# Kernel tuning notes

Hardware: AMD Instinct MI355X
Metric: run time of the kernel (lower is better)

The kernel has to match this reference:

```python
import jax, jax.numpy as jnp
import numpy as np

D_MODEL = 768
D_STATE = 16
B, L = 4, 2048


def setup_inputs() -> dict:
    key = jax.random.key(0)
    ks = jax.random.split(key, 8)
    s = 1.0 / np.sqrt(D_MODEL)
    x = jax.random.normal(ks[0], (B, L, D_MODEL), jnp.float32)
    W_in = jax.random.normal(ks[1], (D_MODEL, 2 * D_MODEL), jnp.float32) * s
    b_in = jnp.zeros((2 * D_MODEL,), jnp.float32)
    W_B = jax.random.normal(ks[2], (D_MODEL, D_STATE), jnp.float32) * s
    b_B = jnp.zeros((D_STATE,), jnp.float32)
    W_C = jax.random.normal(ks[3], (D_MODEL, D_STATE), jnp.float32) * s
    b_C = jnp.zeros((D_STATE,), jnp.float32)
    W_delta = jax.random.normal(ks[4], (D_MODEL, D_MODEL), jnp.float32) * s
    b_delta = jnp.zeros((D_MODEL,), jnp.float32)
    W_out = jax.random.normal(ks[5], (D_MODEL, D_MODEL), jnp.float32) * s
    b_out = jnp.zeros((D_MODEL,), jnp.float32)
    # A_log init from the module: log(A + 1) with A[s, d] = s+1
    A_log = jnp.log(jnp.arange(1, D_STATE + 1, dtype=jnp.float32)[:, None]
                    * jnp.ones((1, D_MODEL), jnp.float32) + 1.0)
    D = jnp.ones((D_MODEL,), jnp.float32)
    return {"x": x, "W_in": W_in, "b_in": b_in, "W_B": W_B, "b_B": b_B,
            "W_C": W_C, "b_C": b_C, "W_delta": W_delta, "b_delta": b_delta,
            "W_out": W_out, "b_out": b_out, "A_log": A_log, "D": D}


def reference(x, W_in, b_in, W_B, b_B, W_C, b_C, W_delta, b_delta,
              W_out, b_out, A_log, D):
    x_proj = x @ W_in + b_in                      # (B, L, 2*d_model)
    x_main, x_gate = jnp.split(x_proj, 2, axis=-1)
    x_main = jax.nn.silu(x_main)
    B_mat = x_main @ W_B + b_B                    # (B, L, d_state)
    C_mat = x_main @ W_C + b_C                    # (B, L, d_state)
    delta = jax.nn.softplus(x_main @ W_delta + b_delta) + 0.0001
    delta = jnp.clip(delta, 0.0001, 1.0)          # (B, L, d_model)
    A = jnp.clip(-jnp.exp(A_log), -5.0, -0.1)     # (d_state, d_model)
    deltaA = jnp.exp(jnp.clip(delta[:, :, None, :] * A[None, None, :, :], -2.0, 0.0))
    deltaA = jnp.clip(deltaA, 0.05, 1.0)          # (B, L, d_state, d_model)
    deltaB_u = jnp.clip(delta[:, :, None, :] * B_mat[:, :, :, None] * x_main[:, :, None, :],
                        -5.0, 5.0)                # (B, L, d_state, d_model)

    def binary_operator(elem1, elem2):
        A1, Bu1 = elem1
        A2, Bu2 = elem2
        A_c = jnp.clip(A2 * A1, 1e-06, 10.0)
        Bu_c = jnp.clip(A2 * Bu1 + Bu2, -100.0, 100.0)
        return (A_c, Bu_c)

    # elementwise combine => scanning along axis=1 of the batched arrays is
    # identical to vmapping a per-batch scan over axis 0
    _, h_Bu = jax.lax.associative_scan(binary_operator, (deltaA, deltaB_u), axis=1)
    y = jnp.einsum('blsd,bls->bld', h_Bu, C_mat)
    y = jnp.clip(y, -10.0, 10.0)
    y = y + x_main * D[None, None, :]
    y = y * jax.nn.silu(x_gate)
    y = jnp.clip(y @ W_out + b_out, -10.0, 10.0)
    return y
```

## Files before the change

kernel.cpp:

```cpp
#include <hip/hip_runtime.h>
#include <hip/hip_bf16.h>
#include <cstdint>
#include <cstddef>

#define D_MODEL 768
#define D_STATE 16
#define BB      4
#define LL      2048
#define M_TOT   (BB*LL)
#define NCHUNK  64
#define LCH     (LL/NCHUNK)
#define N_DBC   896

typedef __attribute__((ext_vector_type(8))) short bf16x8;
typedef __attribute__((ext_vector_type(4))) float f32x4;

__device__ __forceinline__ float clampf_(float x, float lo, float hi) {
    return fminf(fmaxf(x, lo), hi);
}
__device__ __forceinline__ float siluf_(float x) {
    return x / (1.f + __expf(-x));
}
__device__ __forceinline__ unsigned short f2bf(float f) {
    unsigned u = __float_as_uint(f);
    u += 0x7fffu + ((u >> 16) & 1u);
    return (unsigned short)(u >> 16);
}
__device__ __forceinline__ float bf2f(unsigned short u) {
    return __uint_as_float(((unsigned)u) << 16);
}
__device__ __forceinline__ void gload16(void* lds, const void* g) {
    __builtin_amdgcn_global_load_lds(
        (const __attribute__((address_space(1))) void*)g,
        (__attribute__((address_space(3))) void*)lds, 16, 0, 0);
}


__global__ __launch_bounds__(256) void k_convert_x(const float* __restrict__ x,
                                                   unsigned short* __restrict__ xb, int n4) {
    int i = blockIdx.x * 256 + threadIdx.x;
    if (i >= n4) return;
    float4 v = ((const float4*)x)[i];
    ushort4 o;
    o.x = f2bf(v.x); o.y = f2bf(v.y); o.z = f2bf(v.z); o.w = f2bf(v.w);
    ((ushort4*)xb)[i] = o;
}

__global__ __launch_bounds__(256) void k_prep_A(const float* __restrict__ A_log,
                                                float* __restrict__ A_cl, int n) {
    int i = blockIdx.x * 256 + threadIdx.x;
    if (i < n) A_cl[i] = clampf_(-__expf(A_log[i]), -5.f, -0.1f);
}

__global__ __launch_bounds__(256) void k_transpose_bf16(const float* __restrict__ src,
                                                        unsigned short* __restrict__ dst,
                                                        int R, int C) {
    __shared__ float tile[32][33];
    int tx = threadIdx.x & 31, ty = threadIdx.x >> 5;
    int c0 = blockIdx.x * 32, r0 = blockIdx.y * 32;
    #pragma unroll
    for (int rr = ty; rr < 32; rr += 8)
        tile[rr][tx] = src[(size_t)(r0 + rr) * C + c0 + tx];
    __syncthreads();
    #pragma unroll
    for (int rr = ty; rr < 32; rr += 8)
        dst[(size_t)(c0 + rr) * R + r0 + tx] = f2bf(tile[tx][rr]);
}

__global__ __launch_bounds__(256) void k_fill_bc(const float* __restrict__ W_B,
                                                 const float* __restrict__ W_C,
                                                 unsigned short* __restrict__ WdBC) {
    int idx = blockIdx.x * 256 + threadIdx.x;
    if (idx >= 128 * D_MODEL) return;
    int r = idx / D_MODEL + D_MODEL, k = idx % D_MODEL;
    unsigned short v = 0;
    if (r < D_MODEL + 16)       v = f2bf(W_B[k * 16 + (r - D_MODEL)]);
    else if (r < D_MODEL + 32)  v = f2bf(W_C[k * 16 + (r - D_MODEL - 16)]);
    WdBC[(size_t)r * D_MODEL + k] = v;
}

__global__ __launch_bounds__(256) void k_bias_dbc(const float* __restrict__ b_delta,
                                                  const float* __restrict__ b_B,
                                                  const float* __restrict__ b_C,
                                                  float* __restrict__ bias) {
    int i = blockIdx.x * 256 + threadIdx.x;
    if (i >= N_DBC) return;
    float v = 0.f;
    if (i < D_MODEL)            v = b_delta[i];
    else if (i < D_MODEL + 16)  v = b_B[i - D_MODEL];
    else if (i < D_MODEL + 32)  v = b_C[i - D_MODEL - 16];
    bias[i] = v;
}

template<int EPI>
__global__ __launch_bounds__(256) void k_gemm(const unsigned short* __restrict__ A,
                                              const unsigned short* __restrict__ Bt,
                                              const float* __restrict__ bias,
                                              int K, int gx,
                                              float* __restrict__ out_f,
                                              float* __restrict__ out_f2,
                                              unsigned short* __restrict__ out_b0,
                                              unsigned short* __restrict__ out_b1) {
    __shared__ __align__(16) unsigned short As[2][128 * 32];
    __shared__ __align__(16) unsigned short Bs[2][128 * 32];
    const int tid = threadIdx.x;
    const int wave = tid >> 6, lane = tid & 63;
    const int wm = wave >> 1, wn = wave & 1;

    const int nwg = gridDim.x;
    const int wg = blockIdx.x;
    int swz = wg;
    if ((nwg & 7) == 0) {
        const int q = nwg >> 3;
        swz = (wg & 7) * q + (wg >> 3);
    }
    const int bx = swz % gx, by = swz / gx;
    const int m0 = by * 128, n0 = bx * 128;
    const int lr = lane & 15, lk = (lane >> 4) * 8;

    f32x4 acc[4][4] = {};

    auto stage = [&](int buf, int kt) {
        #pragma unroll
        for (int p = 0; p < 2; ++p) {
            int ci = p * 256 + wave * 64 + lane;
            int row = ci >> 2, k8 = (ci & 3) * 8;
            gload16(&As[buf][(p * 256 + wave * 64) * 8],
                    &A [(size_t)(m0 + row) * K + kt + k8]);
            gload16(&Bs[buf][(p * 256 + wave * 64) * 8],
                    &Bt[(size_t)(n0 + row) * K + kt + k8]);
        }
    };
    auto compute = [&](int buf) {
        bf16x8 af[4], bfr[4];
        #pragma unroll
        for (int mt = 0; mt < 4; ++mt)
            af[mt] = *(const bf16x8*)&As[buf][(wm * 64 + mt * 16 + lr) * 32 + lk];
        #pragma unroll
        for (int nt = 0; nt < 4; ++nt)
            bfr[nt] = *(const bf16x8*)&Bs[buf][(wn * 64 + nt * 16 + lr) * 32 + lk];
        #pragma unroll
        for (int mt = 0; mt < 4; ++mt)
            #pragma unroll
            for (int nt = 0; nt < 4; ++nt)
                acc[mt][nt] = __builtin_amdgcn_mfma_f32_16x16x32_bf16(
                    af[mt], bfr[nt], acc[mt][nt], 0, 0, 0);
    };

    stage(0, 0);
    __syncthreads();
    int cur = 0;
    for (int kt = 32; kt < K; kt += 32) {
        stage(cur ^ 1, kt);
        compute(cur);
        __syncthreads();
        cur ^= 1;
    }
    compute(cur);

    #pragma unroll
    for (int mt = 0; mt < 4; ++mt) {
        int row = m0 + wm * 64 + mt * 16 + (lane >> 4) * 4;
        #pragma unroll
        for (int nt = 0; nt < 4; ++nt) {
            int col = n0 + wn * 64 + nt * 16 + (lane & 15);
            #pragma unroll
            for (int i = 0; i < 4; ++i) {
                int r = row + i;
                float v = acc[mt][nt][i] + bias[col];
                if (EPI == 0) {
                    float s = siluf_(v);
                    if (col < D_MODEL) out_b0[(size_t)r * D_MODEL + col] = f2bf(s);
                    else               out_b1[(size_t)r * D_MODEL + (col - D_MODEL)] = f2bf(s);
                } else if (EPI == 1) {
                    if (col < D_MODEL) {
                        float sp = (v > 20.f) ? v : log1pf(__expf(v));
                        out_b0[(size_t)r * D_MODEL + col] = f2bf(clampf_(sp + 1e-4f, 1e-4f, 1.f));
                    } else if (col < D_MODEL + 16) {
                        out_f[(size_t)r * D_STATE + (col - D_MODEL)] = v;
                    } else if (col < D_MODEL + 32) {
                        out_f2[(size_t)r * D_STATE + (col - D_MODEL - 16)] = v;
                    }
                } else {
                    out_f[(size_t)r * D_MODEL + col] = clampf_(v, -10.f, 10.f);
                }
            }
        }
    }
}

__global__ __launch_bounds__(256) void k_scanA(const unsigned short* __restrict__ dlt,
                                               const unsigned short* __restrict__ xm,
                                               const float* __restrict__ Bm,
                                               const float* __restrict__ A_cl,
                                               float* __restrict__ h_end,
                                               float* __restrict__ Aprod) {
    const int d = blockIdx.x * 256 + threadIdx.x;
    const int c = blockIdx.y, b = blockIdx.z;
    __shared__ float Bsh[LCH][D_STATE];
    const int rowbase = b * LL + c * LCH;
    for (int i = threadIdx.x; i < LCH * D_STATE; i += 256)
        ((float*)Bsh)[i] = Bm[(size_t)rowbase * D_STATE + i];
    __syncthreads();

    float Asv[16], h[16], ap[16];
    #pragma unroll
    for (int s = 0; s < 16; ++s) {
        Asv[s] = A_cl[s * D_MODEL + d];
        h[s] = 0.f; ap[s] = 1.f;
    }
    for (int tt = 0; tt < LCH; ++tt) {
        const size_t rowoff = (size_t)(rowbase + tt);
        float dltv = bf2f(dlt[rowoff * D_MODEL + d]);
        float xv   = bf2f(xm [rowoff * D_MODEL + d]);
        float dx = dltv * xv;
        #pragma unroll
        for (int s = 0; s < 16; ++s) {
            float dA  = __expf(fmaxf(dltv * Asv[s], -2.f));
            float dBu = clampf_(dx * Bsh[tt][s], -5.f, 5.f);
            h[s] = clampf_(fmaf(dA, h[s], dBu), -100.f, 100.f);
            ap[s] *= dA;
        }
    }
    const size_t off = (((size_t)b * NCHUNK + c) * D_STATE) * D_MODEL + d;
    #pragma unroll
    for (int s = 0; s < 16; ++s) {
        h_end[off + (size_t)s * D_MODEL] = h[s];
        Aprod[off + (size_t)s * D_MODEL] = ap[s];
    }
}

__global__ __launch_bounds__(256) void k_scanB(const float* __restrict__ h_end,
                                               const float* __restrict__ Aprod,
                                               float* __restrict__ h_in) {
    const int idx = blockIdx.x * 256 + threadIdx.x;
    const int d = idx % D_MODEL;
    const int rest = idx / D_MODEL;
    const int s = rest & 15, b = rest >> 4;
    float hc = 0.f;
    for (int c = 0; c < NCHUNK; ++c) {
        const size_t off = (((size_t)b * NCHUNK + c) * D_STATE + s) * D_MODEL + d;
        h_in[off] = hc;
        hc = Aprod[off] * hc + h_end[off];
    }
}

__global__ __launch_bounds__(256) void k_scanC(const unsigned short* __restrict__ dlt,
                                               const unsigned short* __restrict__ xm,
                                               const float* __restrict__ Bm,
                                               const float* __restrict__ Cm,
                                               const float* __restrict__ A_cl,
                                               const float* __restrict__ h_in,
                                               const float* __restrict__ Dvec,
                                               const unsigned short* __restrict__ gate,
                                               unsigned short* __restrict__ ymid) {
    const int d = blockIdx.x * 256 + threadIdx.x;
    const int c = blockIdx.y, b = blockIdx.z;
    __shared__ float Bsh[LCH][D_STATE];
    __shared__ float Csh[LCH][D_STATE];
    const int rowbase = b * LL + c * LCH;
    for (int i = threadIdx.x; i < LCH * D_STATE; i += 256) {
        ((float*)Bsh)[i] = Bm[(size_t)rowbase * D_STATE + i];
        ((float*)Csh)[i] = Cm[(size_t)rowbase * D_STATE + i];
    }
    __syncthreads();

    float Asv[16], h[16];
    const size_t coff = (((size_t)b * NCHUNK + c) * D_STATE) * D_MODEL + d;
    #pragma unroll
    for (int s = 0; s < 16; ++s) {
        Asv[s] = A_cl[s * D_MODEL + d];
        h[s] = h_in[coff + (size_t)s * D_MODEL];
    }
    const float Dv = Dvec[d];
    for (int tt = 0; tt < LCH; ++tt) {
        const size_t rowoff = (size_t)(rowbase + tt);
        float dltv = bf2f(dlt[rowoff * D_MODEL + d]);
        float xv   = bf2f(xm [rowoff * D_MODEL + d]);
        float dx = dltv * xv;
        float y = 0.f;
        #pragma unroll
        for (int s = 0; s < 16; ++s) {
            float dA  = __expf(fmaxf(dltv * Asv[s], -2.f));
            float dBu = clampf_(dx * Bsh[tt][s], -5.f, 5.f);
            h[s] = clampf_(fmaf(dA, h[s], dBu), -100.f, 100.f);
            y = fmaf(h[s], Csh[tt][s], y);
        }
        y = clampf_(y, -10.f, 10.f);
        y = fmaf(xv, Dv, y);
        y *= bf2f(gate[rowoff * D_MODEL + d]);
        ymid[rowoff * D_MODEL + d] = f2bf(y);
    }
}

extern "C" void kernel_launch(void* const* d_in, const int* in_sizes, int n_in,
                              void* d_out, int out_size, void* d_ws, size_t ws_size,
                              hipStream_t stream) {
    const float* x       = (const float*)d_in[0];
    const float* W_in    = (const float*)d_in[1];
    const float* b_in    = (const float*)d_in[2];
    const float* W_B     = (const float*)d_in[3];
    const float* b_B     = (const float*)d_in[4];
    const float* W_C     = (const float*)d_in[5];
    const float* b_C     = (const float*)d_in[6];
    const float* W_delta = (const float*)d_in[7];
    const float* b_delta = (const float*)d_in[8];
    const float* W_out   = (const float*)d_in[9];
    const float* b_out   = (const float*)d_in[10];
    const float* A_log   = (const float*)d_in[11];
    const float* Dvec    = (const float*)d_in[12];
    float* out = (float*)d_out;

    char* p = (char*)d_ws;
    auto alloc = [&](size_t bytes) {
        char* r = p;
        p += (bytes + 255) & ~(size_t)255;
        return r;
    };
    unsigned short* xb    = (unsigned short*)alloc((size_t)M_TOT * D_MODEL * 2);
    unsigned short* Wint  = (unsigned short*)alloc((size_t)2 * D_MODEL * D_MODEL * 2);
    unsigned short* WdBC  = (unsigned short*)alloc((size_t)N_DBC * D_MODEL * 2);
    unsigned short* Wot   = (unsigned short*)alloc((size_t)D_MODEL * D_MODEL * 2);
    float*          bdbc  = (float*)alloc((size_t)N_DBC * 4);
    unsigned short* xm_b  = (unsigned short*)alloc((size_t)M_TOT * D_MODEL * 2);
    unsigned short* gate_b= (unsigned short*)alloc((size_t)M_TOT * D_MODEL * 2);
    unsigned short* dlt_b = (unsigned short*)alloc((size_t)M_TOT * D_MODEL * 2);
    float*          Bm    = (float*)alloc((size_t)M_TOT * D_STATE * 4);
    float*          Cm    = (float*)alloc((size_t)M_TOT * D_STATE * 4);
    float*          A_cl  = (float*)alloc((size_t)D_STATE * D_MODEL * 4);
    float*          h_end = (float*)alloc((size_t)BB * NCHUNK * D_STATE * D_MODEL * 4);
    float*          Aprod = (float*)alloc((size_t)BB * NCHUNK * D_STATE * D_MODEL * 4);
    float*          h_in  = (float*)alloc((size_t)BB * NCHUNK * D_STATE * D_MODEL * 4);
    unsigned short* ymid  = (unsigned short*)alloc((size_t)M_TOT * D_MODEL * 2);

    k_convert_x<<<(M_TOT * D_MODEL / 4 + 255) / 256, 256, 0, stream>>>(x, xb, M_TOT * D_MODEL / 4);
    k_prep_A<<<(D_STATE * D_MODEL + 255) / 256, 256, 0, stream>>>(A_log, A_cl, D_STATE * D_MODEL);
    k_transpose_bf16<<<dim3(2 * D_MODEL / 32, D_MODEL / 32), 256, 0, stream>>>(W_in, Wint, D_MODEL, 2 * D_MODEL);
    k_transpose_bf16<<<dim3(D_MODEL / 32, D_MODEL / 32), 256, 0, stream>>>(W_delta, WdBC, D_MODEL, D_MODEL);
    k_fill_bc<<<(128 * D_MODEL + 255) / 256, 256, 0, stream>>>(W_B, W_C, WdBC);
    k_bias_dbc<<<(N_DBC + 255) / 256, 256, 0, stream>>>(b_delta, b_B, b_C, bdbc);
    k_transpose_bf16<<<dim3(D_MODEL / 32, D_MODEL / 32), 256, 0, stream>>>(W_out, Wot, D_MODEL, D_MODEL);

    k_gemm<0><<<dim3((2 * D_MODEL / 128) * (M_TOT / 128)), 256, 0, stream>>>(
        xb, Wint, b_in, D_MODEL, 2 * D_MODEL / 128, nullptr, nullptr, xm_b, gate_b);
    k_gemm<1><<<dim3((N_DBC / 128) * (M_TOT / 128)), 256, 0, stream>>>(
        xm_b, WdBC, bdbc, D_MODEL, N_DBC / 128, Bm, Cm, dlt_b, nullptr);
    k_scanA<<<dim3(D_MODEL / 256, NCHUNK, BB), 256, 0, stream>>>(dlt_b, xm_b, Bm, A_cl, h_end, Aprod);
    k_scanB<<<(BB * D_STATE * D_MODEL) / 256, 256, 0, stream>>>(h_end, Aprod, h_in);
    k_scanC<<<dim3(D_MODEL / 256, NCHUNK, BB), 256, 0, stream>>>(
        dlt_b, xm_b, Bm, Cm, A_cl, h_in, Dvec, gate_b, ymid);
    k_gemm<2><<<dim3((D_MODEL / 128) * (M_TOT / 128)), 256, 0, stream>>>(
        ymid, Wot, b_out, D_MODEL, D_MODEL / 128, out, nullptr, nullptr, nullptr);
}
```

Measured before the change: 214.9 us.

## Triple-buffer GEMM LDS staging with explicit vmcnt waits and precomputed load pointers

Moves the bf16 MFMA GEMM from a double-buffered to a three-stage LDS pipeline. Two tiles ahead are kept in flight and explicit s_waitcnt vmcnt/lgkmcnt plus s_barrier calls replace __syncthreads. Global load addresses are precomputed once so the staging code does less per-iteration address arithmetic. The goal is to hide global-load latency behind MFMA compute. In exchange LDS use grows by half, which may reduce occupancy, and correctness now depends on hand-counted vmcnt values matching the gload16 instruction count.

Result: no change. 212.5 us (-1.1%).

```diff
diff --git a/kernel.cpp b/kernel.cpp
--- a/kernel.cpp
+++ b/kernel.cpp
@@ -101,8 +101,8 @@
                                               float* __restrict__ out_f2,
                                               unsigned short* __restrict__ out_b0,
                                               unsigned short* __restrict__ out_b1) {
-    __shared__ __align__(16) unsigned short As[2][128 * 32];
-    __shared__ __align__(16) unsigned short Bs[2][128 * 32];
+    __shared__ __align__(16) unsigned short As[3][128 * 32];
+    __shared__ __align__(16) unsigned short Bs[3][128 * 32];
     const int tid = threadIdx.x;
     const int wave = tid >> 6, lane = tid & 63;
     const int wm = wave >> 1, wn = wave & 1;
@@ -117,19 +117,24 @@
     const int bx = swz % gx, by = swz / gx;
     const int m0 = by * 128, n0 = bx * 128;
     const int lr = lane & 15, lk = (lane >> 4) * 8;
+    const int NT = K >> 5;
+
+    const int ci0 = wave * 64 + lane;
+    const int ci1 = 256 + ci0;
+    const unsigned short* ga0 = &A [(size_t)(m0 + (ci0 >> 2)) * K + (ci0 & 3) * 8];
+    const unsigned short* ga1 = &A [(size_t)(m0 + (ci1 >> 2)) * K + (ci1 & 3) * 8];
+    const unsigned short* gb0 = &Bt[(size_t)(n0 + (ci0 >> 2)) * K + (ci0 & 3) * 8];
+    const unsigned short* gb1 = &Bt[(size_t)(n0 + (ci1 >> 2)) * K + (ci1 & 3) * 8];
+    const int ldsOff0 = (wave * 64) * 8;
+    const int ldsOff1 = (256 + wave * 64) * 8;
 
     f32x4 acc[4][4] = {};
 
     auto stage = [&](int buf, int kt) {
-        #pragma unroll
-        for (int p = 0; p < 2; ++p) {
-            int ci = p * 256 + wave * 64 + lane;
-            int row = ci >> 2, k8 = (ci & 3) * 8;
-            gload16(&As[buf][(p * 256 + wave * 64) * 8],
-                    &A [(size_t)(m0 + row) * K + kt + k8]);
-            gload16(&Bs[buf][(p * 256 + wave * 64) * 8],
-                    &Bt[(size_t)(n0 + row) * K + kt + k8]);
-        }
+        gload16(&As[buf][ldsOff0], ga0 + kt);
+        gload16(&As[buf][ldsOff1], ga1 + kt);
+        gload16(&Bs[buf][ldsOff0], gb0 + kt);
+        gload16(&Bs[buf][ldsOff1], gb1 + kt);
     };
     auto compute = [&](int buf) {
         bf16x8 af[4], bfr[4];
@@ -148,15 +153,31 @@
     };
 
     stage(0, 0);
-    __syncthreads();
-    int cur = 0;
-    for (int kt = 32; kt < K; kt += 32) {
-        stage(cur ^ 1, kt);
-        compute(cur);
-        __syncthreads();
-        cur ^= 1;
-    }
-    compute(cur);
+    stage(1, 32);
+    stage(2, 64);
+    asm volatile("s_waitcnt vmcnt(8)" ::: "memory");
+    __builtin_amdgcn_sched_barrier(0);
+    __builtin_amdgcn_s_barrier();
+
+    for (int t = 0; t < NT - 3; ++t) {
+        compute(t % 3);
+        asm volatile("s_waitcnt lgkmcnt(0)" ::: "memory");
+        __builtin_amdgcn_sched_barrier(0);
+        __builtin_amdgcn_s_barrier();
+        stage(t % 3, (t + 3) << 5);
+        asm volatile("s_waitcnt vmcnt(8)" ::: "memory");
+        __builtin_amdgcn_sched_barrier(0);
+        __builtin_amdgcn_s_barrier();
+    }
+    compute((NT - 3) % 3);
+    asm volatile("s_waitcnt vmcnt(4)" ::: "memory");
+    __builtin_amdgcn_sched_barrier(0);
+    __builtin_amdgcn_s_barrier();
+    compute((NT - 2) % 3);
+    asm volatile("s_waitcnt vmcnt(0)" ::: "memory");
+    __builtin_amdgcn_sched_barrier(0);
+    __builtin_amdgcn_s_barrier();
+    compute((NT - 1) % 3);
 
     #pragma unroll
     for (int mt = 0; mt < 4; ++mt) {
```
